# Performance work log

Hardware: AMD Instinct MI355X
Metric: run time of the kernel (lower is better)

## Reference

```python
import jax, jax.numpy as jnp
import numpy as np


def setup_inputs() -> dict:
    key = jax.random.key(0)
    ks = jax.random.split(key, 8)
    C, G, F = 500, 200, 500          # cells_oi, genes_oi, position bins (fragmentprob_size)
    N_GENES, N_CLUST = 1000, 10      # total genes, clusters
    NFRAG = 5_000_000
    bincounts = jax.random.randint(ks[0], (G, F), 0, 20).astype(jnp.float32)
    baseline_weight = jax.random.normal(ks[1], (N_GENES, F), jnp.float32) * 0.1
    differential_weight = jax.random.normal(ks[2], (N_CLUST, 1, 1), jnp.float32) * 0.01
    cluster_modifier = jax.random.normal(ks[3], (N_CLUST,), jnp.float32) * 0.01
    genes_oi = jax.random.randint(ks[4], (G,), 0, N_GENES)
    labels = jax.random.randint(ks[5], (C,), 0, N_CLUST)
    local_cellxgene_ix = jax.random.randint(ks[6], (NFRAG,), 0, C * G)
    binix = jax.random.randint(ks[7], (NFRAG,), 0, F)
    return dict(bincounts=bincounts, baseline_weight=baseline_weight,
                differential_weight=differential_weight, cluster_modifier=cluster_modifier,
                genes_oi=genes_oi, labels=labels,
                local_cellxgene_ix=local_cellxgene_ix, binix=binix)


def reference(bincounts, baseline_weight, differential_weight, cluster_modifier,
              genes_oi, labels, local_cellxgene_ix, binix):
    G, F = bincounts.shape
    C = labels.shape[0]
    # predictor2 is Identity, final_channels = n_hidden_dims = 1
    gene_embedding = bincounts[:, :, None]                     # [G, F, 1]
    baseline = baseline_weight[genes_oi]                       # [G, F]
    cell_embedding = differential_weight[labels][:, :, 0]      # [C, 1]
    # matmul([1,G,F,H], [C,1,H,1]).squeeze(-1) -> [C,G,F]
    u = (jnp.einsum('gfh,ch->cgf', gene_embedding, cell_embedding)
         + baseline[None]
         + cluster_modifier[labels][:, None, None])            # [C, G, F]
    # histogram of fragments into (cell x gene x bin)
    idx = local_cellxgene_ix * F + binix
    count = jnp.zeros(C * G * F, dtype=u.dtype).at[idx].add(1.0).reshape(C, G, F)
    # Poisson(rate=exp(u)).log_prob(count) = count*u - exp(u) - lgamma(count+1)
    logp = count * u - jnp.exp(u) - jax.lax.lgamma(count + 1.0)
    return logp.sum(-1)                                        # [C, G]
```

## Files before the change

kernel.cpp:

```cpp
#include <hip/hip_runtime.h>
#include <stdint.h>

#define C_   500
#define G_   200
#define F_   500
#define K_   10
#define CG_  (C_ * G_)
#define CGPB 125
#define NBUCK (CG_ / CGPB)
#define RSTRIDE 504
#define WPR  (RSTRIDE / 8)
#define NCW2 (CGPB * WPR + 1)
#define TPB_P 1024
#define GRID_P 512
#define NBLK 512
#define TPB_B 512
#define CHUNK_MAX 10240
#define FPT2 (CHUNK_MAX / TPB_P / 2)
#define SLOT 32
#define OVF_CAP 32

__constant__ float LGF[16] = {
    0.0f, 0.0f, 0.69314718f, 1.79175947f, 3.17805383f, 4.78749174f,
    6.57925121f, 8.52516136f, 10.60460290f, 12.80182748f, 15.10441257f,
    17.50230785f, 19.98721450f, 22.55216385f, 25.19122118f, 27.89927138f
};

__global__ __launch_bounds__(TPB_P) void partition_kernel(
        const int* __restrict__ lci,
        const int* __restrict__ binix,
        const float* __restrict__ bc,
        const float* __restrict__ bw,
        const int* __restrict__ genes_oi,
        const float* __restrict__ dw,
        const float* __restrict__ cm,
        uint16_t* __restrict__ frag16,
        uint16_t* __restrict__ cnt16,
        uint32_t* __restrict__ ovfn,
        uint32_t* __restrict__ ovfe,
        float* __restrict__ u_tab,
        float* __restrict__ E,
        int NF, int chunk) {
    __shared__ uint16_t smem16[NBUCK * SLOT];
    __shared__ uint32_t hist[NBUCK];
    __shared__ float    psum[4];
    __shared__ uint32_t ovf_lds[OVF_CAP];
    __shared__ uint32_t oc;
    int tid = threadIdx.x;
    int blk = blockIdx.x;
    int s0 = blk * chunk;
    int s1 = min(s0 + chunk, NF);
    int nloc = s1 - s0;

    if (tid < NBUCK) hist[tid] = 0;
    if (tid < 4) psum[tid] = 0.0f;
    if (tid == 0) oc = 0u;
    __syncthreads();

    {
        int p = blk * 4 + (tid >> 8);
        if (p < K_ * G_) {
            int sub = tid & 255;
            int k = p / G_;
            int g = p - k * G_;
            float dwk = dw[k];
            float cmk = cm[k];
            const float* bcg = bc + (size_t)g * F_;
            const float* bwg = bw + (size_t)genes_oi[g] * F_;
            float* urow = u_tab + (size_t)p * F_;
            float u0 = dwk * bcg[sub] + bwg[sub] + cmk;
            urow[sub] = u0;
            float s = __expf(u0);
            int f1 = sub + 256;
            if (f1 < F_) {
                float u1 = dwk * bcg[f1] + bwg[f1] + cmk;
                urow[f1] = u1;
                s += __expf(u1);
            }
#pragma unroll
            for (int off = 32; off > 0; off >>= 1) s += __shfl_down(s, off);
            if ((tid & 63) == 0) atomicAdd(&psum[tid >> 8], s);
        }
    }

    const int2* lci2 = (const int2*)(lci + s0);
    const int2* bin2 = (const int2*)(binix + s0);
#pragma unroll
    for (int u = 0; u < FPT2; ++u) {
        int pi = u * TPB_P + tid;
        int e0 = pi * 2;
        if (e0 + 1 < nloc) {
            int2 cg2 = lci2[pi];
            int2 f2  = bin2[pi];
            {
                uint32_t b  = (uint32_t)cg2.x / CGPB;
                uint32_t lp = ((uint32_t)cg2.x - b * CGPB) * RSTRIDE + (uint32_t)f2.x;
                uint32_t r  = atomicAdd(&hist[b], 1u);
                if (r < SLOT) smem16[b * SLOT + r] = (uint16_t)lp;
                else {
                    uint32_t o = atomicAdd(&oc, 1u);
                    if (o < OVF_CAP) ovf_lds[o] = (b << 16) | lp;
                }
            }
            {
                uint32_t b  = (uint32_t)cg2.y / CGPB;
                uint32_t lp = ((uint32_t)cg2.y - b * CGPB) * RSTRIDE + (uint32_t)f2.y;
                uint32_t r  = atomicAdd(&hist[b], 1u);
                if (r < SLOT) smem16[b * SLOT + r] = (uint16_t)lp;
                else {
                    uint32_t o = atomicAdd(&oc, 1u);
                    if (o < OVF_CAP) ovf_lds[o] = (b << 16) | lp;
                }
            }
        } else if (e0 < nloc) {
            int cg = lci[s0 + e0];
            int f  = binix[s0 + e0];
            uint32_t b  = (uint32_t)cg / CGPB;
            uint32_t lp = ((uint32_t)cg - b * CGPB) * RSTRIDE + (uint32_t)f;
            uint32_t r  = atomicAdd(&hist[b], 1u);
            if (r < SLOT) smem16[b * SLOT + r] = (uint16_t)lp;
            else {
                uint32_t o = atomicAdd(&oc, 1u);
                if (o < OVF_CAP) ovf_lds[o] = (b << 16) | lp;
            }
        }
    }
    __syncthreads();

    if (tid < 4) {
        int p = blk * 4 + tid;
        if (p < K_ * G_) E[p] = psum[tid];
    }
    if (tid < NBUCK)
        cnt16[(size_t)blk * NBUCK + tid] = (uint16_t)min(hist[tid], (uint32_t)SLOT);

    const uint4* s4 = (const uint4*)smem16;
    for (int i = tid; i < NBUCK * 4; i += TPB_P) {
        int seg = i >> 2;
        int q   = i & 3;
        uint32_t n = min(hist[seg], (uint32_t)SLOT);
        if ((uint32_t)(q * 8) < n) {
            uint4* dst = (uint4*)(frag16 + ((size_t)seg * NBLK + blk) * SLOT);
            dst[q] = s4[i];
        }
    }

    if (tid == 0) ovfn[blk] = min(oc, (uint32_t)OVF_CAP);
    if (tid < OVF_CAP && tid < oc) ovfe[blk * OVF_CAP + tid] = ovf_lds[tid];
}

__global__ __launch_bounds__(TPB_B) void bucket_kernel(
        const uint16_t* __restrict__ frag16,
        const uint16_t* __restrict__ cnt16,
        const uint32_t* __restrict__ ovfn,
        const uint32_t* __restrict__ ovfe,
        const float* __restrict__ u_tab,
        const float* __restrict__ E,
        const int* __restrict__ labels,
        float* __restrict__ out) {
    __shared__ uint32_t cnt[NCW2];
    __shared__ uint16_t cnts[NBLK];
    __shared__ int pairidx[CGPB];
    int b = blockIdx.x;
    int tid = threadIdx.x;

    uint4* c4 = (uint4*)cnt;
    for (int w = tid; w < NCW2 / 4; w += TPB_B) c4[w] = make_uint4(0u, 0u, 0u, 0u);
    if (tid < CGPB) {
        int cg = b * CGPB + tid;
        int c = cg / G_;
        int g = cg - c * G_;
        pairidx[tid] = labels[c] * G_ + g;
    }
    if (tid < NBLK) cnts[tid] = cnt16[(size_t)tid * NBUCK + b];
    __syncthreads();

    const uint4* fb4 = (const uint4*)(frag16 + (size_t)b * NBLK * SLOT);
    for (int i = tid; i < NBLK * 4; i += TPB_B) {
        uint32_t blkq = (uint32_t)i >> 2;
        uint32_t q    = (uint32_t)i & 3u;
        int n  = (int)cnts[blkq];
        int j0 = (int)q * 8;
        if (j0 < n) {
            uint4 four = fb4[i];
            int m = n - j0;
            uint32_t wq[4] = {four.x, four.y, four.z, four.w};
#pragma unroll
            for (int t = 0; t < 8; ++t) {
                if (t < m) {
                    uint32_t l = (wq[t >> 1] >> ((t & 1) * 16)) & 0xFFFFu;
                    atomicAdd(&cnt[l >> 3], 1u << ((l & 7u) * 4u));
                }
            }
        }
    }
    if (tid < NBLK) {
        uint32_t on = ovfn[tid];
        for (uint32_t q = 0; q < on; ++q) {
            uint32_t e = ovfe[tid * OVF_CAP + q];
            if ((e >> 16) == (uint32_t)b) {
                uint32_t l = e & 0xFFFFu;
                atomicAdd(&cnt[l >> 3], 1u << ((l & 7u) * 4u));
            }
        }
    }
    __syncthreads();

    int wave = tid >> 6, lane = tid & 63;
    for (int r = wave; r < CGPB; r += (TPB_B / 64)) {
        float s = 0.0f;
        if (lane < WPR) {
            uint32_t v = cnt[r * WPR + lane];
            if (v) {
                const float4* up = (const float4*)(u_tab + (size_t)pairidx[r] * F_ + 8 * lane);
                float4 ua = up[0];
                float4 ub = up[1];
                s += (float)( v        & 0xFu) * ua.x
                   + (float)((v >> 4)  & 0xFu) * ua.y
                   + (float)((v >> 8)  & 0xFu) * ua.z
                   + (float)((v >> 12) & 0xFu) * ua.w
                   + (float)((v >> 16) & 0xFu) * ub.x
                   + (float)((v >> 20) & 0xFu) * ub.y
                   + (float)((v >> 24) & 0xFu) * ub.z
                   + (float)((v >> 28)       ) * ub.w;
                if (v & 0xEEEEEEEEu) {
#pragma unroll
                    for (int q = 0; q < 8; ++q)
                        s -= LGF[(v >> (q * 4)) & 0xFu];
                }
            }
        }
#pragma unroll
        for (int off = 32; off > 0; off >>= 1) s += __shfl_down(s, off);
        if (lane == 0) out[b * CGPB + r] = s - E[pairidx[r]];
    }
}

extern "C" void kernel_launch(void* const* d_in, const int* in_sizes, int n_in,
                              void* d_out, int out_size, void* d_ws, size_t ws_size,
                              hipStream_t stream) {
    const float* bc     = (const float*)d_in[0];
    const float* bw     = (const float*)d_in[1];
    const float* dw     = (const float*)d_in[2];
    const float* cm     = (const float*)d_in[3];
    const int* genes_oi = (const int*)d_in[4];
    const int* labels   = (const int*)d_in[5];
    const int* lci      = (const int*)d_in[6];
    const int* binix    = (const int*)d_in[7];
    float* out = (float*)d_out;

    const int NF = in_sizes[6];
    int chunk = (NF + GRID_P - 1) / GRID_P;
    chunk = (chunk + 1) & ~1;
    if (chunk > CHUNK_MAX) chunk = CHUNK_MAX;

    char* ws = (char*)d_ws;
    size_t off_cnt16 = ((size_t)NBUCK * NBLK * SLOT * sizeof(uint16_t) + 255) & ~(size_t)255;
    size_t off_ovfn  = (off_cnt16 + (size_t)NBLK * NBUCK * sizeof(uint16_t) + 255) & ~(size_t)255;
    size_t off_ovfe  = (off_ovfn + NBLK * sizeof(uint32_t) + 255) & ~(size_t)255;
    size_t off_utab  = (off_ovfe + (size_t)NBLK * OVF_CAP * sizeof(uint32_t) + 255) & ~(size_t)255;
    size_t off_E     = (off_utab + ((size_t)K_ * G_ * F_ + 16) * sizeof(float) + 255) & ~(size_t)255;

    uint16_t* frag16 = (uint16_t*)ws;
    uint16_t* cnt16  = (uint16_t*)(ws + off_cnt16);
    uint32_t* ovfn   = (uint32_t*)(ws + off_ovfn);
    uint32_t* ovfe   = (uint32_t*)(ws + off_ovfe);
    float*    u_tab  = (float*)(ws + off_utab);
    float*    E      = (float*)(ws + off_E);

    partition_kernel<<<GRID_P, TPB_P, 0, stream>>>(
        lci, binix, bc, bw, genes_oi, dw, cm,
        frag16, cnt16, ovfn, ovfe, u_tab, E, NF, chunk);

    bucket_kernel<<<NBUCK, TPB_B, 0, stream>>>(
        frag16, cnt16, ovfn, ovfe, u_tab, E, labels, out);
}
```

Measured before the change: 126.3 us.

## Accumulate Poisson log-prob incrementally per fragment instead of per-bin reduction pass

The bucket kernel now computes each row's sum on the fly. Every fragment insertion uses the atomic's returned old count to add u minus log(old+1), which telescopes to count*u - lgamma(count+1). This replaces the second pass that scanned the packed 4-bit count words and did a wave reduction per row. The row stride becomes a power of two (512) so the local index splits with shifts. The cost is a scattered global u_tab load and a float LDS atomic for every fragment, plus non-deterministic float summation order.

Result: slower. 145.1 us (+14.9%).

```diff
diff --git a/kernel.cpp b/kernel.cpp
--- a/kernel.cpp
+++ b/kernel.cpp
@@ -8,9 +8,9 @@
 #define CG_  (C_ * G_)
 #define CGPB 125
 #define NBUCK (CG_ / CGPB)
-#define RSTRIDE 504
-#define WPR  (RSTRIDE / 8)
-#define NCW2 (CGPB * WPR + 1)
+#define RSTRIDE 512
+#define WPRW 64
+#define NCW  (CGPB * WPRW)
 #define TPB_P 1024
 #define GRID_P 512
 #define NBLK 512
@@ -19,12 +19,7 @@
 #define FPT2 (CHUNK_MAX / TPB_P / 2)
 #define SLOT 32
 #define OVF_CAP 32
-
-__constant__ float LGF[16] = {
-    0.0f, 0.0f, 0.69314718f, 1.79175947f, 3.17805383f, 4.78749174f,
-    6.57925121f, 8.52516136f, 10.60460290f, 12.80182748f, 15.10441257f,
-    17.50230785f, 19.98721450f, 22.55216385f, 25.19122118f, 27.89927138f
-};
+#define LN2F 0.69314718f
 
 __global__ __launch_bounds__(TPB_P) void partition_kernel(
         const int* __restrict__ lci,
@@ -94,7 +89,7 @@
             int2 f2  = bin2[pi];
             {
                 uint32_t b  = (uint32_t)cg2.x / CGPB;
-                uint32_t lp = ((uint32_t)cg2.x - b * CGPB) * RSTRIDE + (uint32_t)f2.x;
+                uint32_t lp = (((uint32_t)cg2.x - b * CGPB) << 9) | (uint32_t)f2.x;
                 uint32_t r  = atomicAdd(&hist[b], 1u);
                 if (r < SLOT) smem16[b * SLOT + r] = (uint16_t)lp;
                 else {
@@ -104,7 +99,7 @@
             }
             {
                 uint32_t b  = (uint32_t)cg2.y / CGPB;
-                uint32_t lp = ((uint32_t)cg2.y - b * CGPB) * RSTRIDE + (uint32_t)f2.y;
+                uint32_t lp = (((uint32_t)cg2.y - b * CGPB) << 9) | (uint32_t)f2.y;
                 uint32_t r  = atomicAdd(&hist[b], 1u);
                 if (r < SLOT) smem16[b * SLOT + r] = (uint16_t)lp;
                 else {
@@ -116,7 +111,7 @@
             int cg = lci[s0 + e0];
             int f  = binix[s0 + e0];
             uint32_t b  = (uint32_t)cg / CGPB;
-            uint32_t lp = ((uint32_t)cg - b * CGPB) * RSTRIDE + (uint32_t)f;
+            uint32_t lp = (((uint32_t)cg - b * CGPB) << 9) | (uint32_t)f;
             uint32_t r  = atomicAdd(&hist[b], 1u);
             if (r < SLOT) smem16[b * SLOT + r] = (uint16_t)lp;
             else {
@@ -158,19 +153,21 @@
         const float* __restrict__ E,
         const int* __restrict__ labels,
         float* __restrict__ out) {
-    __shared__ uint32_t cnt[NCW2];
+    __shared__ uint32_t cnt[NCW];
     __shared__ uint16_t cnts[NBLK];
-    __shared__ int pairidx[CGPB];
+    __shared__ int   pairidx[CGPB];
+    __shared__ float rowsum[CGPB];
     int b = blockIdx.x;
     int tid = threadIdx.x;
 
     uint4* c4 = (uint4*)cnt;
-    for (int w = tid; w < NCW2 / 4; w += TPB_B) c4[w] = make_uint4(0u, 0u, 0u, 0u);
+    for (int w = tid; w < NCW / 4; w += TPB_B) c4[w] = make_uint4(0u, 0u, 0u, 0u);
     if (tid < CGPB) {
         int cg = b * CGPB + tid;
         int c = cg / G_;
         int g = cg - c * G_;
         pairidx[tid] = labels[c] * G_ + g;
+        rowsum[tid] = 0.0f;
     }
     if (tid < NBLK) cnts[tid] = cnt16[(size_t)tid * NBUCK + b];
     __syncthreads();
@@ -188,8 +185,15 @@
 #pragma unroll
             for (int t = 0; t < 8; ++t) {
                 if (t < m) {
-                    uint32_t l = (wq[t >> 1] >> ((t & 1) * 16)) & 0xFFFFu;
-                    atomicAdd(&cnt[l >> 3], 1u << ((l & 7u) * 4u));
+                    uint32_t l  = (wq[t >> 1] >> ((t & 1) * 16)) & 0xFFFFu;
+                    uint32_t sh = (l & 7u) * 4u;
+                    uint32_t w  = atomicAdd(&cnt[l >> 3], 1u << sh);
+                    uint32_t o  = (w >> sh) & 0xFu;
+                    uint32_t rw = l >> 9;
+                    uint32_t f  = l & 511u;
+                    float uv = u_tab[(size_t)pairidx[rw] * F_ + f];
+                    float dl = __log2f((float)(o + 1u)) * LN2F;
+                    atomicAdd(&rowsum[rw], uv - dl);
                 }
             }
         }
@@ -199,41 +203,21 @@
         for (uint32_t q = 0; q < on; ++q) {
             uint32_t e = ovfe[tid * OVF_CAP + q];
             if ((e >> 16) == (uint32_t)b) {
-                uint32_t l = e & 0xFFFFu;
-                atomicAdd(&cnt[l >> 3], 1u << ((l & 7u) * 4u));
-            }
-        }
-    }
-    __syncthreads();
-
-    int wave = tid >> 6, lane = tid & 63;
-    for (int r = wave; r < CGPB; r += (TPB_B / 64)) {
-        float s = 0.0f;
-        if (lane < WPR) {
-            uint32_t v = cnt[r * WPR + lane];
-            if (v) {
-                const float4* up = (const float4*)(u_tab + (size_t)pairidx[r] * F_ + 8 * lane);
-                float4 ua = up[0];
-                float4 ub = up[1];
-                s += (float)( v        & 0xFu) * ua.x
-                   + (float)((v >> 4)  & 0xFu) * ua.y
-                   + (float)((v >> 8)  & 0xFu) * ua.z
-                   + (float)((v >> 12) & 0xFu) * ua.w
-                   + (float)((v >> 16) & 0xFu) * ub.x
-                   + (float)((v >> 20) & 0xFu) * ub.y
-                   + (float)((v >> 24) & 0xFu) * ub.z
-                   + (float)((v >> 28)       ) * ub.w;
-                if (v & 0xEEEEEEEEu) {
-#pragma unroll
-                    for (int q = 0; q < 8; ++q)
-                        s -= LGF[(v >> (q * 4)) & 0xFu];
-                }
-            }
-        }
-#pragma unroll
-        for (int off = 32; off > 0; off >>= 1) s += __shfl_down(s, off);
-        if (lane == 0) out[b * CGPB + r] = s - E[pairidx[r]];
-    }
+                uint32_t l  = e & 0xFFFFu;
+                uint32_t sh = (l & 7u) * 4u;
+                uint32_t w  = atomicAdd(&cnt[l >> 3], 1u << sh);
+                uint32_t o  = (w >> sh) & 0xFu;
+                uint32_t rw = l >> 9;
+                uint32_t f  = l & 511u;
+                float uv = u_tab[(size_t)pairidx[rw] * F_ + f];
+                float dl = __log2f((float)(o + 1u)) * LN2F;
+                atomicAdd(&rowsum[rw], uv - dl);
+            }
+        }
+    }
+    __syncthreads();
+
+    if (tid < CGPB) out[b * CGPB + tid] = rowsum[tid] - E[pairidx[tid]];
 }
 
 extern "C" void kernel_launch(void* const* d_in, const int* in_sizes, int n_in,
```
